# Optimization experiments

Measured on AMD Instinct MI355X. Metric: run time of the kernel, lower is better.

## Reference

```python
import jax, jax.numpy as jnp
import numpy as np

N, E, G = 50000, 640000, 1024
D, RD, H = 128, 200, 512
NUM_ATOM_FEATS, ATOM_VOCAB = 9, 64
NUM_BOND_FEATS, BOND_VOCAB = 3, 16


def setup_inputs() -> dict:
    key = jax.random.key(0)
    ks = jax.random.split(key, 24)
    inp = {
        "x_feat": jax.random.randint(ks[0], (N, NUM_ATOM_FEATS), 0, ATOM_VOCAB),
        "edge_index": jax.random.randint(ks[1], (2, E), 0, N),
        "edge_attr_feat": jax.random.randint(ks[2], (E, NUM_BOND_FEATS), 0, BOND_VOCAB),
        "batch": jnp.sort(jax.random.randint(ks[3], (N,), 0, G)),
        "rdkit_feats": jax.random.normal(ks[4], (G, RD), dtype=jnp.float32),
        # learned params
        "atom_emb": jax.random.normal(ks[5], (NUM_ATOM_FEATS, ATOM_VOCAB, D), dtype=jnp.float32) * 0.02,
        "bond_emb": jax.random.normal(ks[6], (NUM_BOND_FEATS, BOND_VOCAB, D), dtype=jnp.float32) * 0.02,
        "conv1_w1": jax.random.normal(ks[7], (D, D), dtype=jnp.float32) / np.sqrt(D),
        "conv1_b1": jnp.zeros((D,), jnp.float32),
        "conv1_w2": jax.random.normal(ks[8], (D, D), dtype=jnp.float32) / np.sqrt(D),
        "conv1_b2": jnp.zeros((D,), jnp.float32),
        "conv2_w1": jax.random.normal(ks[9], (D, D), dtype=jnp.float32) / np.sqrt(D),
        "conv2_b1": jnp.zeros((D,), jnp.float32),
        "conv2_w2": jax.random.normal(ks[10], (D, D), dtype=jnp.float32) / np.sqrt(D),
        "conv2_b2": jnp.zeros((D,), jnp.float32),
        "mlp_w1": jax.random.normal(ks[11], (D + RD, H), dtype=jnp.float32) / np.sqrt(D + RD),
        "mlp_b1": jnp.zeros((H,), jnp.float32),
        "mlp_w2": jax.random.normal(ks[12], (H, H // 2), dtype=jnp.float32) / np.sqrt(H),
        "mlp_b2": jnp.zeros((H // 2,), jnp.float32),
        "mlp_w3": jax.random.normal(ks[13], (H // 2, 1), dtype=jnp.float32) / np.sqrt(H // 2),
        "mlp_b3": jnp.zeros((1,), jnp.float32),
    }
    return inp


def _gine_conv(x, edge_index, edge_attr, w1, b1, w2, b2, eps=0.0):
    # PyG GINEConv: out = nn((1+eps)*x + sum_{j in N(i)} relu(x_j + e_ji))
    src, dst = edge_index[0], edge_index[1]
    msg = jax.nn.relu(x[src] + edge_attr)               # [E, D]
    agg = jax.ops.segment_sum(msg, dst, num_segments=x.shape[0])  # [N, D]
    h = (1.0 + eps) * x + agg
    h = jax.nn.relu(h @ w1 + b1)
    return h @ w2 + b2


def reference(x_feat, edge_index, edge_attr_feat, batch, rdkit_feats,
              atom_emb, bond_emb,
              conv1_w1, conv1_b1, conv1_w2, conv1_b2,
              conv2_w1, conv2_b1, conv2_w2, conv2_b2,
              mlp_w1, mlp_b1, mlp_w2, mlp_b2, mlp_w3, mlp_b3):
    # AtomEncoder / BondEncoder: sum of per-feature categorical embeddings
    x = atom_emb[jnp.arange(NUM_ATOM_FEATS)[None, :], x_feat].sum(axis=1)          # [N, D]
    edge_attr = bond_emb[jnp.arange(NUM_BOND_FEATS)[None, :], edge_attr_feat].sum(axis=1)  # [E, D]

    x = _gine_conv(x, edge_index, edge_attr, conv1_w1, conv1_b1, conv1_w2, conv1_b2)
    x = _gine_conv(x, edge_index, edge_attr, conv2_w1, conv2_b1, conv2_w2, conv2_b2)

    # global mean pool over graphs
    sums = jax.ops.segment_sum(x, batch, num_segments=G)                # [G, D]
    counts = jax.ops.segment_sum(jnp.ones((x.shape[0],), x.dtype), batch, num_segments=G)
    pooled = sums / jnp.maximum(counts, 1.0)[:, None]

    h = jnp.concatenate([pooled, rdkit_feats], axis=1)                  # [G, D+RD]
    h = jax.nn.relu(h @ mlp_w1 + mlp_b1)   # dropout is identity in eval mode
    h = jax.nn.relu(h @ mlp_w2 + mlp_b2)
    return h @ mlp_w3 + mlp_b3                                          # [G, 1]
```

## Files before the change

### kernel.cpp

```cpp
#include <hip/hip_runtime.h>

#define N_NODES 50000
#define N_EDGES 640000
#define N_GRAPH 1024
#define D 128
#define RD 200
#define CAP 64

typedef __attribute__((ext_vector_type(4))) float f32x4;
typedef __attribute__((ext_vector_type(8))) float f32x8;
typedef __attribute__((ext_vector_type(4))) _Float16 half4;
typedef __attribute__((ext_vector_type(8))) _Float16 half8;

__global__ void k_pre(const float* __restrict__ emb,
                      const int* __restrict__ xf, const int* __restrict__ batch,
                      const int* __restrict__ ei, const int* __restrict__ bondf,
                      const float* __restrict__ w0, const float* __restrict__ w1,
                      const float* __restrict__ w2, const float* __restrict__ w3,
                      const float* __restrict__ mw1, const float* __restrict__ mw2,
                      _Float16* __restrict__ cWf,
                      _Float16* __restrict__ W1f,
                      _Float16* __restrict__ W2f,
                      _Float16* __restrict__ x16, int* __restrict__ deg,
                      int2* __restrict__ drep, int* __restrict__ gstart) {
  if (blockIdx.x < 3125) {
    int t = blockIdx.x * 256 + threadIdx.x;
    int node = t >> 4, c = (t & 15) << 3;
    if ((t & 15) == 0) {
      int b = batch[node];
      int prev = (node == 0) ? -1 : batch[node - 1];
      for (int g = prev + 1; g <= b; ++g) gstart[g] = node;
      if (node == N_NODES - 1)
        for (int g = b + 1; g <= N_GRAPH; ++g) gstart[g] = N_NODES;
    }
    int v[9];
#pragma unroll
    for (int f = 0; f < 9; ++f) v[f] = xf[node * 9 + f];
    f32x8 a = (f32x8)(0.f);
#pragma unroll
    for (int f = 0; f < 9; ++f) {
      const float* er = &emb[(size_t)(f * 64 + v[f]) * D + c];
      float4 v0 = *(const float4*)er;
      float4 v1 = *(const float4*)(er + 4);
      a[0] += v0.x; a[1] += v0.y; a[2] += v0.z; a[3] += v0.w;
      a[4] += v1.x; a[5] += v1.y; a[6] += v1.z; a[7] += v1.w;
    }
    half8 o;
#pragma unroll
    for (int tt = 0; tt < 8; ++tt) o[tt] = (_Float16)a[tt];
    *(half8*)&x16[(size_t)node * D + c] = o;
  } else if (blockIdx.x < 5625) {
    int e = (blockIdx.x - 3125) * 256 + threadIdx.x;
    int d = ei[N_EDGES + e];
    int rank = atomicAdd(&deg[d], 1);
    int s = ei[e];
    int f0 = bondf[e * 3], f1 = bondf[e * 3 + 1], f2 = bondf[e * 3 + 2];
    drep[e] = make_int2(d | (rank << 16), s | (f0 << 16) | (f1 << 20) | (f2 << 24));
  } else {
    int u = (blockIdx.x - 5625) * 256 + threadIdx.x;
    if (u < 8192) {
      int mat = u >> 11, r = u & 2047;
      int frag = r >> 6, lane = r & 63;
      int n0 = frag >> 2, kk = frag & 3;
      int n = n0 * 16 + (lane & 15);
      int kb = (lane >> 4) * 8 + kk * 32;
      const float* W = (mat == 0) ? w0 : (mat == 1) ? w1 : (mat == 2) ? w2 : w3;
      half8 o;
#pragma unroll
      for (int j = 0; j < 8; ++j) o[j] = (_Float16)W[(kb + j) * D + n];
      *(half8*)&cWf[((size_t)mat * 2048 + r) * 8] = o;
    } else if (u < 8192 + 22528) {
      int t2 = u - 8192;
      int frag = t2 >> 6, lane = t2 & 63;
      int n0 = frag / 11, kk = frag % 11;
      int n = n0 * 16 + (lane & 15);
      int kb = (lane >> 4) * 8 + kk * 32;
      half8 o;
#pragma unroll
      for (int j = 0; j < 8; ++j) {
        int k = kb + j;
        o[j] = (k < 328) ? (_Float16)mw1[k * 512 + n] : (_Float16)0.f;
      }
      *(half8*)&W1f[(size_t)t2 * 8] = o;
    } else if (u < 8192 + 22528 + 16384) {
      int t2 = u - 8192 - 22528;
      int frag = t2 >> 6, lane = t2 & 63;
      int n0 = frag >> 4, kk = frag & 15;
      int n = n0 * 16 + (lane & 15);
      int kb = (lane >> 4) * 8 + kk * 32;
      half8 o;
#pragma unroll
      for (int j = 0; j < 8; ++j) o[j] = (_Float16)mw2[(kb + j) * 256 + n];
      *(half8*)&W2f[(size_t)t2 * 8] = o;
    }
  }
}

__global__ void k_fill(const int2* __restrict__ drep, int* __restrict__ csr1) {
  int e = blockIdx.x * 256 + threadIdx.x;
  if (e >= N_EDGES) return;
  int2 v = drep[e];
  int d = v.x & 0xFFFF;
  int rank = ((unsigned)v.x) >> 16;
  if (rank < CAP) csr1[(d << 6) | rank] = v.y;
}

__global__ __launch_bounds__(256) void k_agg(
    const _Float16* __restrict__ X, const int* __restrict__ deg,
    const int* __restrict__ csr1, const float* __restrict__ bemb,
    _Float16* __restrict__ out) {
  __shared__ half8 sB[48 * 16];
  for (int t = threadIdx.x; t < 768; t += blockDim.x) {
    float4 v0 = *(const float4*)&bemb[t * 8];
    float4 v1 = *(const float4*)&bemb[t * 8 + 4];
    half8 h;
    h[0] = (_Float16)v0.x; h[1] = (_Float16)v0.y; h[2] = (_Float16)v0.z; h[3] = (_Float16)v0.w;
    h[4] = (_Float16)v1.x; h[5] = (_Float16)v1.y; h[6] = (_Float16)v1.z; h[7] = (_Float16)v1.w;
    sB[t] = h;
  }
  __syncthreads();
  int lane = threadIdx.x & 63;
  int quad = lane >> 4, l15 = lane & 15, c8 = l15 * 8;
  int wid = blockIdx.x * 4 + (threadIdx.x >> 6);
  int nw = gridDim.x * 4;
  if (wid >= N_NODES) return;
  int pdeg = deg[wid];
  int pcreg = csr1[(wid << 6) + lane];
  for (int i = wid; i < N_NODES; i += nw) {
    int degn = pdeg;
    int creg = pcreg;
    int i2 = (i + nw < N_NODES) ? i + nw : i;
    pdeg = deg[i2];
    pcreg = csr1[(i2 << 6) + lane];
    int dq = degn > CAP ? CAP : degn;
    f32x8 ac0 = (f32x8)(0.f), ac1 = (f32x8)(0.f);
    for (int jb = 0; jb < dq; jb += 8) {
      unsigned e0v = (unsigned)__shfl(creg, jb + quad);
      unsigned e1v = (unsigned)__shfl(creg, jb + 4 + quad);
      if (jb + quad < dq) {
        half8 x0 = *(const half8*)&X[(size_t)(e0v & 0xFFFF) * D + c8];
        unsigned p0 = e0v >> 16;
        half8 m0h = (x0 + sB[(p0 & 15) * 16 + l15]) +
                    (sB[256 + ((p0 >> 4) & 15) * 16 + l15] + sB[512 + (p0 >> 8) * 16 + l15]);
        f32x8 g0 = __builtin_convertvector(m0h, f32x8);
#pragma unroll
        for (int tt = 0; tt < 8; ++tt) ac0[tt] += fmaxf(g0[tt], 0.f);
      }
      if (jb + 4 + quad < dq) {
        half8 x1 = *(const half8*)&X[(size_t)(e1v & 0xFFFF) * D + c8];
        unsigned p1 = e1v >> 16;
        half8 m1h = (x1 + sB[(p1 & 15) * 16 + l15]) +
                    (sB[256 + ((p1 >> 4) & 15) * 16 + l15] + sB[512 + (p1 >> 8) * 16 + l15]);
        f32x8 g1 = __builtin_convertvector(m1h, f32x8);
#pragma unroll
        for (int tt = 0; tt < 8; ++tt) ac1[tt] += fmaxf(g1[tt], 0.f);
      }
    }
    f32x8 acc = ac0 + ac1;
#pragma unroll
    for (int tt = 0; tt < 8; ++tt) {
      acc[tt] += __shfl_xor(acc[tt], 16);
      acc[tt] += __shfl_xor(acc[tt], 32);
    }
    if (quad == 0) {
      half8 sr = *(const half8*)&X[(size_t)i * D + c8];
      f32x8 o = __builtin_convertvector(sr, f32x8) + acc;
      half8 oh;
#pragma unroll
      for (int tt = 0; tt < 8; ++tt) oh[tt] = (_Float16)o[tt];
      *(half8*)&out[(size_t)i * D + c8] = oh;
    }
  }
}

__global__ __launch_bounds__(256) void k_conv(
    const _Float16* __restrict__ A,
    const _Float16* __restrict__ W1f, const float* __restrict__ b1,
    const _Float16* __restrict__ W2f, const float* __restrict__ b2,
    _Float16* __restrict__ O16) {
  __shared__ _Float16 sW[2048 * 8];
  __shared__ _Float16 sI[128 * 136];
  int tid = threadIdx.x, w = tid >> 6, lane = tid & 63;
  int m0 = blockIdx.x * 128;
  int col16 = lane & 15, q = lane >> 4;
  for (int t = tid; t < 2048; t += 256)
    *(float4*)&sW[t * 8] = *(const float4*)&W1f[(size_t)t * 8];
  half8 afr[2][4];
#pragma unroll
  for (int f = 0; f < 2; ++f) {
    int row = m0 + w * 32 + f * 16 + col16;
    if (row >= N_NODES) row = N_NODES - 1;
    const _Float16* Ar = A + (size_t)row * D + q * 8;
#pragma unroll
    for (int kk = 0; kk < 4; ++kk) afr[f][kk] = *(const half8*)(Ar + kk * 32);
  }
  __syncthreads();
#pragma unroll
  for (int n0 = 0; n0 < 8; ++n0) {
    f32x4 a0 = {0.f, 0.f, 0.f, 0.f}, a1 = {0.f, 0.f, 0.f, 0.f};
#pragma unroll
    for (int kk = 0; kk < 4; ++kk) {
      half8 b = *(const half8*)&sW[((n0 * 4 + kk) * 64 + lane) * 8];
      a0 = __builtin_amdgcn_mfma_f32_16x16x32_f16(afr[0][kk], b, a0, 0, 0, 0);
      a1 = __builtin_amdgcn_mfma_f32_16x16x32_f16(afr[1][kk], b, a1, 0, 0, 0);
    }
    float bb = b1[n0 * 16 + col16];
#pragma unroll
    for (int r = 0; r < 4; ++r) {
      sI[(w * 32 + q * 4 + r) * 136 + n0 * 16 + col16] = (_Float16)fmaxf(a0[r] + bb, 0.f);
      sI[(w * 32 + 16 + q * 4 + r) * 136 + n0 * 16 + col16] = (_Float16)fmaxf(a1[r] + bb, 0.f);
    }
  }
  __syncthreads();
  for (int t = tid; t < 2048; t += 256)
    *(float4*)&sW[t * 8] = *(const float4*)&W2f[(size_t)t * 8];
  half8 a2[2][4];
#pragma unroll
  for (int f = 0; f < 2; ++f) {
    const _Float16* tr = &sI[(w * 32 + f * 16 + col16) * 136 + q * 8];
#pragma unroll
    for (int kk = 0; kk < 4; ++kk) a2[f][kk] = *(const half8*)(tr + kk * 32);
  }
  __syncthreads();
#pragma unroll
  for (int n0 = 0; n0 < 8; ++n0) {
    f32x4 a0 = {0.f, 0.f, 0.f, 0.f}, a1 = {0.f, 0.f, 0.f, 0.f};
#pragma unroll
    for (int kk = 0; kk < 4; ++kk) {
      half8 b = *(const half8*)&sW[((n0 * 4 + kk) * 64 + lane) * 8];
      a0 = __builtin_amdgcn_mfma_f32_16x16x32_f16(a2[0][kk], b, a0, 0, 0, 0);
      a1 = __builtin_amdgcn_mfma_f32_16x16x32_f16(a2[1][kk], b, a1, 0, 0, 0);
    }
    int col = n0 * 16 + col16;
    float bb = b2[col];
#pragma unroll
    for (int r = 0; r < 4; ++r) {
      int r0 = m0 + w * 32 + q * 4 + r;
      int r1 = r0 + 16;
      if (r0 < N_NODES) O16[(size_t)r0 * D + col] = (_Float16)(a0[r] + bb);
      if (r1 < N_NODES) O16[(size_t)r1 * D + col] = (_Float16)(a1[r] + bb);
    }
  }
}

__global__ __launch_bounds__(512) void k_head(
    const _Float16* __restrict__ x, const int* __restrict__ gstart,
    const float* __restrict__ rdkit,
    const _Float16* __restrict__ W1f, const float* __restrict__ B1,
    const _Float16* __restrict__ W2f, const float* __restrict__ B2,
    const float* __restrict__ W3, const float* __restrict__ B3,
    float* __restrict__ out) {
  __shared__ _Float16 sH[16 * 360];
  __shared__ _Float16 sH1[16 * 520];
  int tid = threadIdx.x, w = tid >> 6, lane = tid & 63;
  int mt = blockIdx.x;
  int col16 = lane & 15, q = lane >> 4;

  for (int t = tid; t < 2880; t += 512) sH[2880 + t] = (_Float16)0.f;

  {
    int row = w;
    int g = mt * 8 + w;
    int half_ = lane >> 5;
    int c4 = (lane & 31) * 4;
    int lo = gstart[g];
    int hi = gstart[g + 1];
    f32x4 a = {0.f, 0.f, 0.f, 0.f};
    for (int i = lo + half_; i < hi; i += 2) {
      half4 v = *(const half4*)&x[(size_t)i * D + c4];
      a += __builtin_convertvector(v, f32x4);
    }
#pragma unroll
    for (int t = 0; t < 4; ++t) a[t] += __shfl_xor(a[t], 32);
    float inv = 1.f / fmaxf((float)(hi - lo), 1.f);
    if (half_ == 0) {
      half4 o;
      o.x = (_Float16)(a[0] * inv); o.y = (_Float16)(a[1] * inv);
      o.z = (_Float16)(a[2] * inv); o.w = (_Float16)(a[3] * inv);
      *(half4*)&sH[row * 360 + c4] = o;
    }
    for (int r = lane; r < RD; r += 64)
      sH[row * 360 + D + r] = (_Float16)rdkit[(size_t)g * RD + r];
    if (lane < 24) sH[row * 360 + 328 + lane] = (_Float16)0.f;
    if (lane == 0) out[g] = B3[0];
  }
  __syncthreads();

  {
    half8 afr[11];
    const _Float16* Ar = &sH[col16 * 360 + q * 8];
#pragma unroll
    for (int kk = 0; kk < 11; ++kk) afr[kk] = *(const half8*)(Ar + kk * 32);
#pragma unroll
    for (int ng = 0; ng < 4; ++ng) {
      int n0 = w * 4 + ng;
      f32x4 acc = {0.f, 0.f, 0.f, 0.f};
#pragma unroll
      for (int kk = 0; kk < 11; ++kk) {
        half8 b = *(const half8*)&W1f[(size_t)((n0 * 11 + kk) * 64 + lane) * 8];
        acc = __builtin_amdgcn_mfma_f32_16x16x32_f16(afr[kk], b, acc, 0, 0, 0);
      }
      int col = n0 * 16 + col16;
      float bb = B1[col];
#pragma unroll
      for (int r = 0; r < 4; ++r)
        sH1[(q * 4 + r) * 520 + col] = (_Float16)fmaxf(acc[r] + bb, 0.f);
    }
  }
  __syncthreads();

  {
    half8 a2[16];
    const _Float16* Ar = &sH1[col16 * 520 + q * 8];
#pragma unroll
    for (int kk = 0; kk < 16; ++kk) a2[kk] = *(const half8*)(Ar + kk * 32);
    float p[4] = {0.f, 0.f, 0.f, 0.f};
#pragma unroll
    for (int ng = 0; ng < 2; ++ng) {
      int n0 = w * 2 + ng;
      f32x4 acc = {0.f, 0.f, 0.f, 0.f};
#pragma unroll
      for (int kk = 0; kk < 16; ++kk) {
        half8 b = *(const half8*)&W2f[(size_t)((n0 * 16 + kk) * 64 + lane) * 8];
        acc = __builtin_amdgcn_mfma_f32_16x16x32_f16(a2[kk], b, acc, 0, 0, 0);
      }
      int col = n0 * 16 + col16;
      float bb = B2[col], w3 = W3[col];
#pragma unroll
      for (int r = 0; r < 4; ++r) p[r] += fmaxf(acc[r] + bb, 0.f) * w3;
    }
#pragma unroll
    for (int r = 0; r < 4; ++r) {
      p[r] += __shfl_xor(p[r], 1);
      p[r] += __shfl_xor(p[r], 2);
      p[r] += __shfl_xor(p[r], 4);
      p[r] += __shfl_xor(p[r], 8);
    }
    if (col16 == 0 && q < 2) {
#pragma unroll
      for (int r = 0; r < 4; ++r)
        atomicAdd(&out[mt * 8 + q * 4 + r], p[r]);
    }
  }
}

extern "C" void kernel_launch(void* const* d_in, const int* in_sizes, int n_in,
                              void* d_out, int out_size, void* d_ws, size_t ws_size,
                              hipStream_t stream) {
  const int* x_feat = (const int*)d_in[0];
  const int* ei = (const int*)d_in[1];
  const int* bondf = (const int*)d_in[2];
  const int* batch = (const int*)d_in[3];
  const float* rdkit = (const float*)d_in[4];
  const float* atom_emb = (const float*)d_in[5];
  const float* bond_emb = (const float*)d_in[6];
  const float* c1w1 = (const float*)d_in[7];
  const float* c1b1 = (const float*)d_in[8];
  const float* c1w2 = (const float*)d_in[9];
  const float* c1b2 = (const float*)d_in[10];
  const float* c2w1 = (const float*)d_in[11];
  const float* c2b1 = (const float*)d_in[12];
  const float* c2w2 = (const float*)d_in[13];
  const float* c2b2 = (const float*)d_in[14];
  const float* mw1 = (const float*)d_in[15];
  const float* mb1 = (const float*)d_in[16];
  const float* mw2 = (const float*)d_in[17];
  const float* mb2 = (const float*)d_in[18];
  const float* mw3 = (const float*)d_in[19];
  const float* mb3 = (const float*)d_in[20];
  float* out = (float*)d_out;

  char* ws = (char*)d_ws;
  size_t off = 0;
  auto alloc = [&](size_t bytes) {
    void* p = ws + off;
    off += (bytes + 255) & ~(size_t)255;
    return p;
  };
  _Float16* x16a = (_Float16*)alloc((size_t)N_NODES * D * 2);
  _Float16* x16b = (_Float16*)alloc((size_t)N_NODES * D * 2);
  _Float16* h16 = (_Float16*)alloc((size_t)N_NODES * D * 2);
  _Float16* x2_16 = (_Float16*)alloc((size_t)N_NODES * D * 2);
  int* deg = (int*)alloc((size_t)N_NODES * 4);
  int* csr1 = (int*)alloc((size_t)N_NODES * CAP * 4);
  int2* drep = (int2*)alloc((size_t)N_EDGES * 8);
  int* gstart = (int*)alloc((size_t)(N_GRAPH + 1) * 4);
  _Float16* cWf = (_Float16*)alloc((size_t)4 * 2048 * 8 * 2);
  _Float16* W1f = (_Float16*)alloc((size_t)352 * 64 * 8 * 2);
  _Float16* W2f = (_Float16*)alloc((size_t)256 * 64 * 8 * 2);

  hipMemsetAsync(deg, 0, (size_t)N_NODES * 4, stream);
  k_pre<<<3125 + 2500 + 196, 256, 0, stream>>>(atom_emb, x_feat, batch,
                                               ei, bondf,
                                               c1w1, c1w2, c2w1, c2w2, mw1, mw2,
                                               cWf, W1f, W2f, x16a, deg, drep,
                                               gstart);
  k_fill<<<(N_EDGES + 255) / 256, 256, 0, stream>>>(drep, csr1);

  int ctiles = (N_NODES + 127) / 128;
  k_agg<<<2048, 256, 0, stream>>>(x16a, deg, csr1, bond_emb, h16);
  k_conv<<<ctiles, 256, 0, stream>>>(h16, cWf + 0 * 16384, c1b1,
                                     cWf + 1 * 16384, c1b2, x16b);
  k_agg<<<2048, 256, 0, stream>>>(x16b, deg, csr1, bond_emb, h16);
  k_conv<<<ctiles, 256, 0, stream>>>(h16, cWf + 2 * 16384, c2b1,
                                     cWf + 3 * 16384, c2b2, x2_16);

  k_head<<<N_GRAPH / 8, 512, 0, stream>>>(x2_16, gstart, rdkit,
                                          W1f, mb1, W2f, mb2, mw3, mb3, out);

  (void)in_sizes; (void)n_in; (void)out_size; (void)ws_size;
}
```

Baseline: 264.6 us.

## Scatter CSR directly in preprocessing, shrink conv tiles, shuffle atom feature loads

The edge pass of k_pre now writes packed source and bond features straight into the capped CSR slot, so the intermediate drep buffer and the separate k_fill launch go away. k_conv now handles 64 rows per block instead of 128, with one 16-row MFMA fragment per wave, which gives more blocks to spread across CUs. Atom feature indices are loaded once per lane and shared across each 16-lane group with shuffles, instead of every thread loading all nine. The smaller conv tile doubles how often each block loads the weights into shared memory, and the CSR writes are now scattered from inside the atomic pass.

```diff
diff --git a/kernel.cpp b/kernel.cpp
--- a/kernel.cpp
+++ b/kernel.cpp
@@ -22,10 +22,11 @@
                       _Float16* __restrict__ W1f,
                       _Float16* __restrict__ W2f,
                       _Float16* __restrict__ x16, int* __restrict__ deg,
-                      int2* __restrict__ drep, int* __restrict__ gstart) {
+                      int* __restrict__ csr1, int* __restrict__ gstart) {
   if (blockIdx.x < 3125) {
     int t = blockIdx.x * 256 + threadIdx.x;
     int node = t >> 4, c = (t & 15) << 3;
+    int lane = threadIdx.x & 63;
     if ((t & 15) == 0) {
       int b = batch[node];
       int prev = (node == 0) ? -1 : batch[node - 1];
@@ -33,13 +34,15 @@
       if (node == N_NODES - 1)
         for (int g = b + 1; g <= N_GRAPH; ++g) gstart[g] = N_NODES;
     }
-    int v[9];
-#pragma unroll
-    for (int f = 0; f < 9; ++f) v[f] = xf[node * 9 + f];
+    int fidx = lane & 15;
+    int myxf = 0;
+    if (fidx < 9) myxf = xf[node * 9 + fidx];
+    int gbase = lane & 48;
     f32x8 a = (f32x8)(0.f);
 #pragma unroll
     for (int f = 0; f < 9; ++f) {
-      const float* er = &emb[(size_t)(f * 64 + v[f]) * D + c];
+      int v = __shfl(myxf, gbase + f);
+      const float* er = &emb[(size_t)(f * 64 + v) * D + c];
       float4 v0 = *(const float4*)er;
       float4 v1 = *(const float4*)(er + 4);
       a[0] += v0.x; a[1] += v0.y; a[2] += v0.z; a[3] += v0.w;
@@ -55,7 +58,8 @@
     int rank = atomicAdd(&deg[d], 1);
     int s = ei[e];
     int f0 = bondf[e * 3], f1 = bondf[e * 3 + 1], f2 = bondf[e * 3 + 2];
-    drep[e] = make_int2(d | (rank << 16), s | (f0 << 16) | (f1 << 20) | (f2 << 24));
+    if (rank < CAP)
+      csr1[(d << 6) | rank] = s | (f0 << 16) | (f1 << 20) | (f2 << 24);
   } else {
     int u = (blockIdx.x - 5625) * 256 + threadIdx.x;
     if (u < 8192) {
@@ -94,15 +98,6 @@
       *(half8*)&W2f[(size_t)t2 * 8] = o;
     }
   }
-}
-
-__global__ void k_fill(const int2* __restrict__ drep, int* __restrict__ csr1) {
-  int e = blockIdx.x * 256 + threadIdx.x;
-  if (e >= N_EDGES) return;
-  int2 v = drep[e];
-  int d = v.x & 0xFFFF;
-  int rank = ((unsigned)v.x) >> 16;
-  if (rank < CAP) csr1[(d << 6) | rank] = v.y;
 }
 
 __global__ __launch_bounds__(256) void k_agg(
@@ -179,66 +174,58 @@
     const _Float16* __restrict__ W2f, const float* __restrict__ b2,
     _Float16* __restrict__ O16) {
   __shared__ _Float16 sW[2048 * 8];
-  __shared__ _Float16 sI[128 * 136];
+  __shared__ _Float16 sI[64 * 136];
   int tid = threadIdx.x, w = tid >> 6, lane = tid & 63;
-  int m0 = blockIdx.x * 128;
+  int m0 = blockIdx.x * 64;
   int col16 = lane & 15, q = lane >> 4;
   for (int t = tid; t < 2048; t += 256)
     *(float4*)&sW[t * 8] = *(const float4*)&W1f[(size_t)t * 8];
-  half8 afr[2][4];
-#pragma unroll
-  for (int f = 0; f < 2; ++f) {
-    int row = m0 + w * 32 + f * 16 + col16;
+  half8 afr[4];
+  {
+    int row = m0 + w * 16 + col16;
     if (row >= N_NODES) row = N_NODES - 1;
     const _Float16* Ar = A + (size_t)row * D + q * 8;
 #pragma unroll
-    for (int kk = 0; kk < 4; ++kk) afr[f][kk] = *(const half8*)(Ar + kk * 32);
+    for (int kk = 0; kk < 4; ++kk) afr[kk] = *(const half8*)(Ar + kk * 32);
   }
   __syncthreads();
 #pragma unroll
   for (int n0 = 0; n0 < 8; ++n0) {
-    f32x4 a0 = {0.f, 0.f, 0.f, 0.f}, a1 = {0.f, 0.f, 0.f, 0.f};
+    f32x4 a0 = {0.f, 0.f, 0.f, 0.f};
 #pragma unroll
     for (int kk = 0; kk < 4; ++kk) {
       half8 b = *(const half8*)&sW[((n0 * 4 + kk) * 64 + lane) * 8];
-      a0 = __builtin_amdgcn_mfma_f32_16x16x32_f16(afr[0][kk], b, a0, 0, 0, 0);
-      a1 = __builtin_amdgcn_mfma_f32_16x16x32_f16(afr[1][kk], b, a1, 0, 0, 0);
+      a0 = __builtin_amdgcn_mfma_f32_16x16x32_f16(afr[kk], b, a0, 0, 0, 0);
     }
     float bb = b1[n0 * 16 + col16];
 #pragma unroll
-    for (int r = 0; r < 4; ++r) {
-      sI[(w * 32 + q * 4 + r) * 136 + n0 * 16 + col16] = (_Float16)fmaxf(a0[r] + bb, 0.f);
-      sI[(w * 32 + 16 + q * 4 + r) * 136 + n0 * 16 + col16] = (_Float16)fmaxf(a1[r] + bb, 0.f);
-    }
+    for (int r = 0; r < 4; ++r)
+      sI[(w * 16 + q * 4 + r) * 136 + n0 * 16 + col16] = (_Float16)fmaxf(a0[r] + bb, 0.f);
   }
   __syncthreads();
   for (int t = tid; t < 2048; t += 256)
     *(float4*)&sW[t * 8] = *(const float4*)&W2f[(size_t)t * 8];
-  half8 a2[2][4];
-#pragma unroll
-  for (int f = 0; f < 2; ++f) {
-    const _Float16* tr = &sI[(w * 32 + f * 16 + col16) * 136 + q * 8];
-#pragma unroll
-    for (int kk = 0; kk < 4; ++kk) a2[f][kk] = *(const half8*)(tr + kk * 32);
+  half8 a2[4];
+  {
+    const _Float16* tr = &sI[(w * 16 + col16) * 136 + q * 8];
+#pragma unroll
+    for (int kk = 0; kk < 4; ++kk) a2[kk] = *(const half8*)(tr + kk * 32);
   }
   __syncthreads();
 #pragma unroll
   for (int n0 = 0; n0 < 8; ++n0) {
-    f32x4 a0 = {0.f, 0.f, 0.f, 0.f}, a1 = {0.f, 0.f, 0.f, 0.f};
+    f32x4 a0 = {0.f, 0.f, 0.f, 0.f};
 #pragma unroll
     for (int kk = 0; kk < 4; ++kk) {
       half8 b = *(const half8*)&sW[((n0 * 4 + kk) * 64 + lane) * 8];
-      a0 = __builtin_amdgcn_mfma_f32_16x16x32_f16(a2[0][kk], b, a0, 0, 0, 0);
-      a1 = __builtin_amdgcn_mfma_f32_16x16x32_f16(a2[1][kk], b, a1, 0, 0, 0);
+      a0 = __builtin_amdgcn_mfma_f32_16x16x32_f16(a2[kk], b, a0, 0, 0, 0);
     }
     int col = n0 * 16 + col16;
     float bb = b2[col];
 #pragma unroll
     for (int r = 0; r < 4; ++r) {
-      int r0 = m0 + w * 32 + q * 4 + r;
-      int r1 = r0 + 16;
+      int r0 = m0 + w * 16 + q * 4 + r;
       if (r0 < N_NODES) O16[(size_t)r0 * D + col] = (_Float16)(a0[r] + bb);
-      if (r1 < N_NODES) O16[(size_t)r1 * D + col] = (_Float16)(a1[r] + bb);
     }
   }
 }
@@ -383,7 +370,6 @@
   _Float16* x2_16 = (_Float16*)alloc((size_t)N_NODES * D * 2);
   int* deg = (int*)alloc((size_t)N_NODES * 4);
   int* csr1 = (int*)alloc((size_t)N_NODES * CAP * 4);
-  int2* drep = (int2*)alloc((size_t)N_EDGES * 8);
   int* gstart = (int*)alloc((size_t)(N_GRAPH + 1) * 4);
   _Float16* cWf = (_Float16*)alloc((size_t)4 * 2048 * 8 * 2);
   _Float16* W1f = (_Float16*)alloc((size_t)352 * 64 * 8 * 2);
@@ -393,11 +379,10 @@
   k_pre<<<3125 + 2500 + 196, 256, 0, stream>>>(atom_emb, x_feat, batch,
                                                ei, bondf,
                                                c1w1, c1w2, c2w1, c2w2, mw1, mw2,
-                                               cWf, W1f, W2f, x16a, deg, drep,
+                                               cWf, W1f, W2f, x16a, deg, csr1,
                                                gstart);
-  k_fill<<<(N_EDGES + 255) / 256, 256, 0, stream>>>(drep, csr1);
-
-  int ctiles = (N_NODES + 127) / 128;
+
+  int ctiles = (N_NODES + 63) / 64;
   k_agg<<<2048, 256, 0, stream>>>(x16a, deg, csr1, bond_emb, h16);
   k_conv<<<ctiles, 256, 0, stream>>>(h16, cWf + 0 * 16384, c1b1,
                                      cWf + 1 * 16384, c1b2, x16b);
```

Result: slower. 279.4 us (+5.6%).
